# Kernel optimization log

Measured on AMD Instinct MI355X. Metric: run time of the kernel, lower is better.

## Reference

```python
import jax, jax.numpy as jnp
from jax import lax
import numpy as np

NBASE = 4
INSIZE = 256
SIZE = NBASE * (2 + 2 * NBASE)  # 40
NTIME, NBATCH = 2000, 128


def crfrle_log_partition(weights, nbase):
    # weights: (ntime, nbatch, 2*nbase*nbase)
    ntime, nbatch, nstate = weights.shape
    eye = jnp.eye(nbase, dtype=weights.dtype)
    ee = jnp.concatenate([eye, eye], axis=1)          # (nbase, 2*nbase)
    holes = -1e30 * ee                                # mask diagonal out for move
    diag = -1e30 * (1.0 - ee)                         # keep only diagonal for stay

    def step(fwd, w_t):
        # fwd: (nbatch, 2*nbase); w_t: (nbatch, 2*nbase*nbase)
        w_mat = w_t.reshape(nbatch, nbase, 2 * nbase)
        ft = fwd[:, None, :]                          # (nbatch, 1, 2*nbase)
        move = jax.scipy.special.logsumexp(ft + w_mat + holes, axis=2)
        stay = jax.scipy.special.logsumexp(ft + w_mat + diag, axis=2)
        return jnp.concatenate([move, stay], axis=1), None

    fwd0 = jnp.zeros((nbatch, 2 * nbase), dtype=weights.dtype)
    fwd, _ = lax.scan(step, fwd0, weights)
    return jax.scipy.special.logsumexp(fwd, axis=1, keepdims=True)  # (nbatch, 1)


def setup_inputs() -> dict:
    key = jax.random.key(0)
    kx, kw, kb = jax.random.split(key, 3)
    x = jax.random.normal(kx, (NTIME, NBATCH, INSIZE), dtype=jnp.float32)
    sd = 0.5 / np.sqrt(INSIZE + SIZE)
    W = sd * jax.random.truncated_normal(kw, -2.0, 2.0, (SIZE, INSIZE), dtype=jnp.float32)
    b = 0.5 * jax.random.truncated_normal(kb, -2.0, 2.0, (SIZE,), dtype=jnp.float32)
    return {"x": x, "W": W, "b": b}


def reference(x, W, b):
    ntime = x.shape[0]
    y = jnp.einsum('tbi,oi->tbo', x, W) + b           # (ntime, nbatch, SIZE)
    shape_p = 1.0 + jax.nn.softplus(y[..., :NBASE])
    scale_p = 0.1 + jax.nn.softplus(y[..., NBASE:2 * NBASE])
    trans = 5.0 * jnp.tanh(y[..., 2 * NBASE:])        # (ntime, nbatch, 2*nbase^2)
    logZ = crfrle_log_partition(trans, NBASE)[None] / ntime  # (1, nbatch, 1)
    return jnp.concatenate([shape_p, scale_p, trans - logZ], axis=2)
```

## Files before the change

### kernel.cpp

```cpp
#include <hip/hip_runtime.h>
#include <hip/hip_bf16.h>

#define NTIME   2000
#define NBATCH  128
#define INSIZE  256
#define NOUT    40
#define NROWS   (NTIME * NBATCH)
#define CCHUNK  80
#define LSTEP   25

typedef __attribute__((ext_vector_type(8))) short  short8;
typedef __attribute__((ext_vector_type(4))) float  float4v;

#define L2E 1.4426950408889634f
#define LN2 0.6931471805599453f

__device__ __forceinline__ float fexp2(float x){ return __builtin_amdgcn_exp2f(x); }
__device__ __forceinline__ float flog2(float x){ return __builtin_amdgcn_logf(x);  }

__device__ __forceinline__ short f2bf(float f) {
    unsigned u = __float_as_uint(f);
    unsigned r = u + 0x7fffu + ((u >> 16) & 1u);
    return (short)(r >> 16);
}

__global__ __launch_bounds__(256) void prep_w(const float* __restrict__ W,
                                              short* __restrict__ Wb)
{
    int idx = blockIdx.x * 256 + threadIdx.x;
    int n = idx >> 8, k = idx & 255;
    float v = (n < NOUT) ? W[n * INSIZE + k] : 0.f;
    Wb[idx] = f2bf(v);
}

__global__ __launch_bounds__(256) void gemm_act(const float* __restrict__ x,
                                                const short* __restrict__ Wb,
                                                const float* __restrict__ bias,
                                                float* __restrict__ out)
{
    const int tid  = threadIdx.x;
    const int wave = tid >> 6, lane = tid & 63;
    const int l16  = lane & 15, quad = lane >> 4;
    const long rowBase = (long)blockIdx.x * 128 + wave * 32;

    float4v acc[2][3];
#pragma unroll
    for (int mi = 0; mi < 2; ++mi)
#pragma unroll
        for (int ni = 0; ni < 3; ++ni)
            acc[mi][ni] = (float4v){0.f, 0.f, 0.f, 0.f};

    const float* xp0 = x + (rowBase + l16) * (long)INSIZE + quad * 8;
    const float* xp1 = xp0 + 16 * INSIZE;
    const short* wp = Wb + l16 * INSIZE + quad * 8;

#pragma unroll
    for (int s = 0; s < 8; ++s) {
        short8 afrag[2];
#pragma unroll
        for (int mi = 0; mi < 2; ++mi) {
            const float* xp = (mi ? xp1 : xp0) + s * 32;
            float4v xa = *(const float4v*)xp;
            float4v xb = *(const float4v*)(xp + 4);
            short8 a;
            a[0] = f2bf(xa[0]); a[1] = f2bf(xa[1]); a[2] = f2bf(xa[2]); a[3] = f2bf(xa[3]);
            a[4] = f2bf(xb[0]); a[5] = f2bf(xb[1]); a[6] = f2bf(xb[2]); a[7] = f2bf(xb[3]);
            afrag[mi] = a;
        }
#pragma unroll
        for (int ni = 0; ni < 3; ++ni) {
            short8 bfrag = *(const short8*)(wp + ni * 16 * INSIZE + s * 32);
            acc[0][ni] = __builtin_amdgcn_mfma_f32_16x16x32_bf16(afrag[0], bfrag, acc[0][ni], 0, 0, 0);
            acc[1][ni] = __builtin_amdgcn_mfma_f32_16x16x32_bf16(afrag[1], bfrag, acc[1][ni], 0, 0, 0);
        }
    }

#pragma unroll
    for (int mi = 0; mi < 2; ++mi) {
        long row0 = rowBase + mi * 16 + quad * 4;
#pragma unroll
        for (int ni = 0; ni < 3; ++ni) {
            int o = ni * 16 + l16;
            if (o >= NOUT) continue;
            float bv = bias[o];
#pragma unroll
            for (int r = 0; r < 4; ++r) {
                float y = acc[mi][ni][r] + bv;
                float val;
                if (o < 8) {
                    float sp = fmaxf(y, 0.f) + LN2 * flog2(1.f + fexp2(-fabsf(y) * L2E));
                    val = (o < 4 ? 1.0f : 0.1f) + sp;
                } else {
                    float e = fexp2(2.f * fabsf(y) * L2E);
                    float t = 1.f - 2.f / (e + 1.f);
                    val = 5.f * copysignf(t, y);
                }
                out[(row0 + r) * NOUT + o] = val;
            }
        }
    }
}

__global__ __launch_bounds__(256) void scan_chunks(const float* __restrict__ out,
                                                   float* __restrict__ chunkM)
{
    const int tid   = threadIdx.x;
    const int g     = tid >> 3, j0 = tid & 7;
    const int c     = blockIdx.x >> 2;
    const int batch = ((blockIdx.x & 3) << 5) + g;
    const int t0    = c * LSTEP;

    float m[8];
#pragma unroll
    for (int i = 0; i < 8; ++i) m[i] = (i == j0) ? 0.f : -1e30f;

    const float* p = out + ((size_t)(t0 * NBATCH + batch) * NOUT + 8);
    float4v w[8];
#pragma unroll
    for (int q = 0; q < 8; ++q) w[q] = *(const float4v*)(p + q * 4);

    for (int step = 0; step < LSTEP; ++step) {
        const float* pn = (step < LSTEP - 1) ? (p + NBATCH * NOUT) : p;
        float4v wn[8];
#pragma unroll
        for (int q = 0; q < 8; ++q) wn[q] = *(const float4v*)(pn + q * 4);

        const float* wv = (const float*)&w[0];
        float nm[8];
#pragma unroll
        for (int i = 0; i < 4; ++i) {
            float s[8];
#pragma unroll
            for (int k = 0; k < 8; ++k) s[k] = fmaf(wv[i * 8 + k], L2E, m[k]);
            float a = s[i], b2 = s[i + 4];
            float mx2 = fmaxf(a, b2), mn2 = fminf(a, b2);
            nm[4 + i] = mx2 + flog2(1.f + fexp2(mn2 - mx2));
            s[i] = -1e30f; s[i + 4] = -1e30f;
            float mx = fmaxf(fmaxf(fmaxf(s[0], s[1]), fmaxf(s[2], s[3])),
                             fmaxf(fmaxf(s[4], s[5]), fmaxf(s[6], s[7])));
            float sum = ((fexp2(s[0] - mx) + fexp2(s[1] - mx)) + (fexp2(s[2] - mx) + fexp2(s[3] - mx)))
                      + ((fexp2(s[4] - mx) + fexp2(s[5] - mx)) + (fexp2(s[6] - mx) + fexp2(s[7] - mx)));
            nm[i] = mx + flog2(sum);
        }
#pragma unroll
        for (int i = 0; i < 8; ++i) m[i] = nm[i];
#pragma unroll
        for (int q = 0; q < 8; ++q) w[q] = wn[q];
        p = pn;
    }

    float* dst = chunkM + (((size_t)batch * CCHUNK + c) * 8 + j0) * 8;
#pragma unroll
    for (int i = 0; i < 8; ++i) dst[i] = m[i];
}

__global__ __launch_bounds__(1024) void combine_k(const float* __restrict__ chunkM,
                                                  float* __restrict__ logZdiv)
{
    const int tid   = threadIdx.x;
    const int ip    = tid & 7;
    const int batch = tid >> 3;
    const int gbase = (tid & 63) & ~7;

    float v[8];
#pragma unroll
    for (int j = 0; j < 8; ++j) v[j] = 0.f;

    for (int c = 0; c < CCHUNK; ++c) {
        const float* Mp = chunkM + (((size_t)batch * CCHUNK + c) << 6);
        float s[8];
#pragma unroll
        for (int j = 0; j < 8; ++j) s[j] = Mp[j * 8 + ip] + v[j];
        float mx = fmaxf(fmaxf(fmaxf(s[0], s[1]), fmaxf(s[2], s[3])),
                         fmaxf(fmaxf(s[4], s[5]), fmaxf(s[6], s[7])));
        float sum = ((fexp2(s[0] - mx) + fexp2(s[1] - mx)) + (fexp2(s[2] - mx) + fexp2(s[3] - mx)))
                  + ((fexp2(s[4] - mx) + fexp2(s[5] - mx)) + (fexp2(s[6] - mx) + fexp2(s[7] - mx)));
        float nv = mx + flog2(sum);
#pragma unroll
        for (int j = 0; j < 8; ++j) v[j] = __shfl(nv, gbase + j, 64);
    }
    float mx = fmaxf(fmaxf(fmaxf(v[0], v[1]), fmaxf(v[2], v[3])),
                     fmaxf(fmaxf(v[4], v[5]), fmaxf(v[6], v[7])));
    float sum = ((fexp2(v[0] - mx) + fexp2(v[1] - mx)) + (fexp2(v[2] - mx) + fexp2(v[3] - mx)))
              + ((fexp2(v[4] - mx) + fexp2(v[5] - mx)) + (fexp2(v[6] - mx) + fexp2(v[7] - mx)));
    float r = mx + flog2(sum);
    if (ip == 0) logZdiv[batch] = r * LN2 / (float)NTIME;
}

__global__ __launch_bounds__(256) void sub_logz(float* __restrict__ out,
                                                const float* __restrict__ logZdiv)
{
    size_t idx = (size_t)blockIdx.x * 256 + threadIdx.x;
    size_t row = idx >> 3;
    int q = (int)(idx & 7);
    int batch = (int)(row & 127);
    float lz = logZdiv[batch];
    float4v* pp = (float4v*)(out + row * NOUT + 8 + q * 4);
    float4v vv = *pp;
    vv[0] -= lz; vv[1] -= lz; vv[2] -= lz; vv[3] -= lz;
    *pp = vv;
}

extern "C" void kernel_launch(void* const* d_in, const int* in_sizes, int n_in,
                              void* d_out, int out_size, void* d_ws, size_t ws_size,
                              hipStream_t stream)
{
    const float* x = (const float*)d_in[0];
    const float* W = (const float*)d_in[1];
    const float* b = (const float*)d_in[2];
    float* out = (float*)d_out;

    char* ws = (char*)d_ws;
    short* Wb      = (short*)ws;
    float* chunkM  = (float*)(ws + 32768);
    float* logZdiv = (float*)(ws + 32768 + (size_t)NBATCH * CCHUNK * 64 * 4);

    hipLaunchKernelGGL(prep_w,      dim3(48),        dim3(256),  0, stream, W, Wb);
    hipLaunchKernelGGL(gemm_act,    dim3(NROWS/128), dim3(256),  0, stream, x, Wb, b, out);
    hipLaunchKernelGGL(scan_chunks, dim3(CCHUNK*4),  dim3(256),  0, stream, out, chunkM);
    hipLaunchKernelGGL(combine_k,   dim3(1),         dim3(1024), 0, stream, chunkM, logZdiv);
    hipLaunchKernelGGL(sub_logz,    dim3(8000),      dim3(256),  0, stream, out, logZdiv);
}
```

Baseline: 448.6 us.

## Fuse CRF chunk scan, combine, and logZ subtraction into one cooperative kernel

Merges the three post-GEMM kernels (chunk scan, combine, subtract) into a single cooperative kernel separated by grid-wide syncs. The combine step becomes per-batch: each of the first 128 blocks loads its batch's chunk matrices into shared memory and does the log-sum-exp reduction with wave shuffles, replacing the old single-block combine. The aim is to remove two launch gaps and to parallelise the serial combine across blocks. In exchange it adds grid.sync overhead, and the subtract pass now runs on only 320 blocks with a grid-stride loop instead of 8000 blocks.

```diff
diff --git a/kernel.cpp b/kernel.cpp
--- a/kernel.cpp
+++ b/kernel.cpp
@@ -1,5 +1,8 @@
 #include <hip/hip_runtime.h>
 #include <hip/hip_bf16.h>
+#include <hip/hip_cooperative_groups.h>
+
+namespace cg = cooperative_groups;
 
 #define NTIME   2000
 #define NBATCH  128
@@ -8,6 +11,7 @@
 #define NROWS   (NTIME * NBATCH)
 #define CCHUNK  80
 #define LSTEP   25
+#define CRFBLK  320
 
 typedef __attribute__((ext_vector_type(8))) short  short8;
 typedef __attribute__((ext_vector_type(4))) float  float4v;
@@ -101,104 +105,123 @@
     }
 }
 
-__global__ __launch_bounds__(256) void scan_chunks(const float* __restrict__ out,
-                                                   float* __restrict__ chunkM)
-{
-    const int tid   = threadIdx.x;
-    const int g     = tid >> 3, j0 = tid & 7;
-    const int c     = blockIdx.x >> 2;
-    const int batch = ((blockIdx.x & 3) << 5) + g;
-    const int t0    = c * LSTEP;
-
-    float m[8];
-#pragma unroll
-    for (int i = 0; i < 8; ++i) m[i] = (i == j0) ? 0.f : -1e30f;
-
-    const float* p = out + ((size_t)(t0 * NBATCH + batch) * NOUT + 8);
-    float4v w[8];
-#pragma unroll
-    for (int q = 0; q < 8; ++q) w[q] = *(const float4v*)(p + q * 4);
-
-    for (int step = 0; step < LSTEP; ++step) {
-        const float* pn = (step < LSTEP - 1) ? (p + NBATCH * NOUT) : p;
-        float4v wn[8];
-#pragma unroll
-        for (int q = 0; q < 8; ++q) wn[q] = *(const float4v*)(pn + q * 4);
-
-        const float* wv = (const float*)&w[0];
-        float nm[8];
-#pragma unroll
-        for (int i = 0; i < 4; ++i) {
-            float s[8];
-#pragma unroll
-            for (int k = 0; k < 8; ++k) s[k] = fmaf(wv[i * 8 + k], L2E, m[k]);
-            float a = s[i], b2 = s[i + 4];
-            float mx2 = fmaxf(a, b2), mn2 = fminf(a, b2);
-            nm[4 + i] = mx2 + flog2(1.f + fexp2(mn2 - mx2));
-            s[i] = -1e30f; s[i + 4] = -1e30f;
-            float mx = fmaxf(fmaxf(fmaxf(s[0], s[1]), fmaxf(s[2], s[3])),
-                             fmaxf(fmaxf(s[4], s[5]), fmaxf(s[6], s[7])));
-            float sum = ((fexp2(s[0] - mx) + fexp2(s[1] - mx)) + (fexp2(s[2] - mx) + fexp2(s[3] - mx)))
-                      + ((fexp2(s[4] - mx) + fexp2(s[5] - mx)) + (fexp2(s[6] - mx) + fexp2(s[7] - mx)));
-            nm[i] = mx + flog2(sum);
-        }
-#pragma unroll
-        for (int i = 0; i < 8; ++i) m[i] = nm[i];
-#pragma unroll
-        for (int q = 0; q < 8; ++q) w[q] = wn[q];
-        p = pn;
-    }
-
-    float* dst = chunkM + (((size_t)batch * CCHUNK + c) * 8 + j0) * 8;
-#pragma unroll
-    for (int i = 0; i < 8; ++i) dst[i] = m[i];
-}
-
-__global__ __launch_bounds__(1024) void combine_k(const float* __restrict__ chunkM,
-                                                  float* __restrict__ logZdiv)
-{
-    const int tid   = threadIdx.x;
-    const int ip    = tid & 7;
-    const int batch = tid >> 3;
-    const int gbase = (tid & 63) & ~7;
-
-    float v[8];
-#pragma unroll
-    for (int j = 0; j < 8; ++j) v[j] = 0.f;
-
-    for (int c = 0; c < CCHUNK; ++c) {
-        const float* Mp = chunkM + (((size_t)batch * CCHUNK + c) << 6);
-        float s[8];
-#pragma unroll
-        for (int j = 0; j < 8; ++j) s[j] = Mp[j * 8 + ip] + v[j];
-        float mx = fmaxf(fmaxf(fmaxf(s[0], s[1]), fmaxf(s[2], s[3])),
-                         fmaxf(fmaxf(s[4], s[5]), fmaxf(s[6], s[7])));
-        float sum = ((fexp2(s[0] - mx) + fexp2(s[1] - mx)) + (fexp2(s[2] - mx) + fexp2(s[3] - mx)))
-                  + ((fexp2(s[4] - mx) + fexp2(s[5] - mx)) + (fexp2(s[6] - mx) + fexp2(s[7] - mx)));
-        float nv = mx + flog2(sum);
-#pragma unroll
-        for (int j = 0; j < 8; ++j) v[j] = __shfl(nv, gbase + j, 64);
-    }
-    float mx = fmaxf(fmaxf(fmaxf(v[0], v[1]), fmaxf(v[2], v[3])),
-                     fmaxf(fmaxf(v[4], v[5]), fmaxf(v[6], v[7])));
-    float sum = ((fexp2(v[0] - mx) + fexp2(v[1] - mx)) + (fexp2(v[2] - mx) + fexp2(v[3] - mx)))
-              + ((fexp2(v[4] - mx) + fexp2(v[5] - mx)) + (fexp2(v[6] - mx) + fexp2(v[7] - mx)));
-    float r = mx + flog2(sum);
-    if (ip == 0) logZdiv[batch] = r * LN2 / (float)NTIME;
-}
-
-__global__ __launch_bounds__(256) void sub_logz(float* __restrict__ out,
-                                                const float* __restrict__ logZdiv)
-{
-    size_t idx = (size_t)blockIdx.x * 256 + threadIdx.x;
-    size_t row = idx >> 3;
-    int q = (int)(idx & 7);
-    int batch = (int)(row & 127);
-    float lz = logZdiv[batch];
-    float4v* pp = (float4v*)(out + row * NOUT + 8 + q * 4);
-    float4v vv = *pp;
-    vv[0] -= lz; vv[1] -= lz; vv[2] -= lz; vv[3] -= lz;
-    *pp = vv;
+__global__ __launch_bounds__(256) void crf_fused(float* __restrict__ out,
+                                                 float* __restrict__ chunkM,
+                                                 float* __restrict__ logZdiv)
+{
+    cg::grid_group grid = cg::this_grid();
+    __shared__ float lds[CCHUNK * 64];
+
+    const int tid = threadIdx.x;
+
+    {
+        const int g     = tid >> 3, j0 = tid & 7;
+        const int c     = blockIdx.x >> 2;
+        const int batch = ((blockIdx.x & 3) << 5) + g;
+        const int t0    = c * LSTEP;
+
+        float m[8];
+#pragma unroll
+        for (int i = 0; i < 8; ++i) m[i] = (i == j0) ? 0.f : -1e30f;
+
+        const float* p = out + ((size_t)(t0 * NBATCH + batch) * NOUT + 8);
+        float4v w[8];
+#pragma unroll
+        for (int q = 0; q < 8; ++q) w[q] = *(const float4v*)(p + q * 4);
+
+        for (int step = 0; step < LSTEP; ++step) {
+            const float* pn = (step < LSTEP - 1) ? (p + NBATCH * NOUT) : p;
+            float4v wn[8];
+#pragma unroll
+            for (int q = 0; q < 8; ++q) wn[q] = *(const float4v*)(pn + q * 4);
+
+            const float* wv = (const float*)&w[0];
+            float nm[8];
+#pragma unroll
+            for (int i = 0; i < 4; ++i) {
+                float s[8];
+#pragma unroll
+                for (int k = 0; k < 8; ++k) s[k] = fmaf(wv[i * 8 + k], L2E, m[k]);
+                float a = s[i], b2 = s[i + 4];
+                float mx2 = fmaxf(a, b2), mn2 = fminf(a, b2);
+                nm[4 + i] = mx2 + flog2(1.f + fexp2(mn2 - mx2));
+                s[i] = -1e30f; s[i + 4] = -1e30f;
+                float mx = fmaxf(fmaxf(fmaxf(s[0], s[1]), fmaxf(s[2], s[3])),
+                                 fmaxf(fmaxf(s[4], s[5]), fmaxf(s[6], s[7])));
+                float sum = ((fexp2(s[0] - mx) + fexp2(s[1] - mx)) + (fexp2(s[2] - mx) + fexp2(s[3] - mx)))
+                          + ((fexp2(s[4] - mx) + fexp2(s[5] - mx)) + (fexp2(s[6] - mx) + fexp2(s[7] - mx)));
+                nm[i] = mx + flog2(sum);
+            }
+#pragma unroll
+            for (int i = 0; i < 8; ++i) m[i] = nm[i];
+#pragma unroll
+            for (int q = 0; q < 8; ++q) w[q] = wn[q];
+            p = pn;
+        }
+
+        float* dst = chunkM + (((size_t)batch * CCHUNK + c) * 8 + j0) * 8;
+#pragma unroll
+        for (int i = 0; i < 8; ++i) dst[i] = m[i];
+    }
+
+    __threadfence();
+    grid.sync();
+
+    if (blockIdx.x < NBATCH) {
+        const int batch = blockIdx.x;
+        const float4v* src = (const float4v*)(chunkM + (size_t)batch * CCHUNK * 64);
+        for (int k = tid; k < CCHUNK * 16; k += 256)
+            ((float4v*)lds)[k] = src[k];
+        __syncthreads();
+
+        if (tid < 64) {
+            const int i  = tid & 7;
+            const int jj = tid >> 3;
+            float v_jj = 0.f;
+            float vnew = 0.f;
+            for (int c = 0; c < CCHUNK; ++c) {
+                float t = lds[c * 64 + jj * 8 + i] + v_jj;
+                float mx = t;
+                mx = fmaxf(mx, __shfl_xor(mx, 8,  64));
+                mx = fmaxf(mx, __shfl_xor(mx, 16, 64));
+                mx = fmaxf(mx, __shfl_xor(mx, 32, 64));
+                float e = fexp2(t - mx);
+                e += __shfl_xor(e, 8,  64);
+                e += __shfl_xor(e, 16, 64);
+                e += __shfl_xor(e, 32, 64);
+                vnew = mx + flog2(e);
+                v_jj = __shfl(vnew, jj, 64);
+            }
+            float t = vnew;
+            float mx = t;
+            mx = fmaxf(mx, __shfl_xor(mx, 1, 64));
+            mx = fmaxf(mx, __shfl_xor(mx, 2, 64));
+            mx = fmaxf(mx, __shfl_xor(mx, 4, 64));
+            float e = fexp2(t - mx);
+            e += __shfl_xor(e, 1, 64);
+            e += __shfl_xor(e, 2, 64);
+            e += __shfl_xor(e, 4, 64);
+            float r = mx + flog2(e);
+            if (tid == 0) logZdiv[batch] = r * LN2 / (float)NTIME;
+        }
+    }
+
+    __threadfence();
+    grid.sync();
+
+    {
+        const size_t total = (size_t)NTIME * NBATCH * 8;
+        for (size_t idx = (size_t)blockIdx.x * 256 + tid; idx < total; idx += (size_t)CRFBLK * 256) {
+            size_t row = idx >> 3;
+            int q = (int)(idx & 7);
+            int batch = (int)(row & 127);
+            float lz = logZdiv[batch];
+            float4v* pp = (float4v*)(out + row * NOUT + 8 + q * 4);
+            float4v vv = *pp;
+            vv[0] -= lz; vv[1] -= lz; vv[2] -= lz; vv[3] -= lz;
+            *pp = vv;
+        }
+    }
 }
 
 extern "C" void kernel_launch(void* const* d_in, const int* in_sizes, int n_in,
@@ -215,9 +238,9 @@
     float* chunkM  = (float*)(ws + 32768);
     float* logZdiv = (float*)(ws + 32768 + (size_t)NBATCH * CCHUNK * 64 * 4);
 
-    hipLaunchKernelGGL(prep_w,      dim3(48),        dim3(256),  0, stream, W, Wb);
-    hipLaunchKernelGGL(gemm_act,    dim3(NROWS/128), dim3(256),  0, stream, x, Wb, b, out);
-    hipLaunchKernelGGL(scan_chunks, dim3(CCHUNK*4),  dim3(256),  0, stream, out, chunkM);
-    hipLaunchKernelGGL(combine_k,   dim3(1),         dim3(1024), 0, stream, chunkM, logZdiv);
-    hipLaunchKernelGGL(sub_logz,    dim3(8000),      dim3(256),  0, stream, out, logZdiv);
-}
+    hipLaunchKernelGGL(prep_w,   dim3(48),         dim3(256), 0, stream, W, Wb);
+    hipLaunchKernelGGL(gemm_act, dim3(NROWS/128),  dim3(256), 0, stream, x, Wb, b, out);
+
+    void* args[] = { (void*)&out, (void*)&chunkM, (void*)&logZdiv };
+    hipLaunchCooperativeKernel((const void*)crf_fused, dim3(CRFBLK), dim3(256), args, 0, stream);
+}
```

After: 569.4 us. 26.9% more time.
